# Performance work log

Hardware: AMD Instinct MI355X
Metric: run time of the kernel (lower is better)

The kernel has to match this reference:

```python
import jax, jax.numpy as jnp
import numpy as np

N, C_IN, C_OUT, V = 4, 64, 64, 8192

def setup_inputs() -> dict:
    key = jax.random.key(0)
    k1, k2, k3, k4 = jax.random.split(key, 4)
    x = jax.random.normal(k1, (N, C_IN, 1, V), dtype=jnp.float32)
    A = jax.random.uniform(k2, (N, V, V), dtype=jnp.float32)
    W = jax.random.normal(k3, (C_OUT, C_IN, 1, 1), dtype=jnp.float32) * 0.05
    b = jax.random.normal(k4, (C_OUT,), dtype=jnp.float32) * 0.05
    return {"x": x, "A": A, "W": W, "b": b}

def reference(x, A, W, b):
    # nn.Conv2d with (1,1) kernel == per-position channel mixing (pointwise GEMM).
    # x: (N, C_in, 1, V) -> squeeze T dim -> (N, C_in, V)
    xs = x[:, :, 0, :]
    y = jnp.einsum('ncv,oc->nov', xs, W[:, :, 0, 0]) + b[None, :, None]  # (N, C_out, V)
    # graph aggregation with per-sample adjacency: torch.einsum('ncv,nvw->ncw', x, A)
    out = jnp.einsum('ncv,nvw->ncw', y, A)  # (N, C_out, V)
    return out, A
```

## Files before the change

kernel.cpp:

```cpp
#include <hip/hip_runtime.h>
#include <stdint.h>

#define NB 4
#define CC 64
#define VV 8192
#define WBK 64
#define KB 64
#define NCHUNK (VV / KB)

typedef float  f32x4  __attribute__((ext_vector_type(4)));
typedef uint32_t u32x2 __attribute__((ext_vector_type(2)));
typedef uint32_t u32x4 __attribute__((ext_vector_type(4)));
typedef __bf16 bf16x8 __attribute__((ext_vector_type(8)));

__device__ __forceinline__ int swz_idx(int row, int v) {
    return row * KB + ((((v >> 3) ^ row) & 7) << 3) + (v & 7);
}

__device__ __forceinline__ uint32_t pkbf(float a, float b) {
    union { __bf16 h[2]; uint32_t u; } t;
    t.h[0] = (__bf16)a; t.h[1] = (__bf16)b;
    return t.u;
}

__device__ __forceinline__ bf16x8 mkfrag(const __bf16* p, int row, int k0) {
    u32x2 lo = *(const u32x2*)(p + swz_idx(row, k0));
    u32x2 hi = *(const u32x2*)(p + swz_idx(row, k0 + 16));
    u32x4 u; u.x = lo.x; u.y = lo.y; u.z = hi.x; u.w = hi.y;
    return __builtin_bit_cast(bf16x8, u);
}

__global__ __launch_bounds__(256) void k_y(const float* __restrict__ x,
                                           const float* __restrict__ Wg,
                                           const float* __restrict__ bg,
                                           __bf16* __restrict__ yws) {
    const int blk = blockIdx.x;
    const int cg  = blk & 3;
    const int vg  = (blk >> 2) * 256 + threadIdx.x;
    const int n   = vg >> 13;
    const int v   = vg & (VV - 1);
    const float* xg = x + (size_t)n * CC * VV + v;

    float acc[16];
    #pragma unroll
    for (int i = 0; i < 16; ++i) acc[i] = bg[cg * 16 + i];

    for (int cp = 0; cp < CC; ++cp) {
        float xv = xg[(size_t)cp * VV];
        #pragma unroll
        for (int i = 0; i < 16; ++i)
            acc[i] += Wg[(cg * 16 + i) * CC + cp] * xv;
    }
    const int t  = v >> 6;
    const int vv = v & 63;
    __bf16* ydst = yws + (size_t)(n * NCHUNK + t) * CC * KB;
    #pragma unroll
    for (int i = 0; i < 16; ++i)
        ydst[swz_idx(cg * 16 + i, vv)] = (__bf16)acc[i];
}

__global__ __launch_bounds__(512, 4) void k_main(const float* __restrict__ A,
                                                 const __bf16* __restrict__ yws,
                                                 float* __restrict__ out,
                                                 float* __restrict__ Acopy,
                                                 int skipTail) {
    __shared__ __attribute__((aligned(16))) __bf16 a_sh[2][WBK * KB];
    __shared__ __attribute__((aligned(16))) __bf16 y_sh[2][CC * KB];

    const int tid = threadIdx.x;
    const int n   = blockIdx.x >> 7;
    const int w0  = (blockIdx.x & 127) * WBK;

    const int wl = tid & 63;
    const int vq = tid >> 6;

    const float* pA = A     + (size_t)n * VV * VV + (size_t)vq * 8 * VV + w0 + wl;
    float*       pC = Acopy + (size_t)n * VV * VV + (size_t)vq * 8 * VV + w0 + wl;
    const uint4* ysrc = (const uint4*)(yws + (size_t)n * NCHUNK * CC * KB);

    const int lane = tid & 63;
    const int wv   = tid >> 6;
    const int mrow = wv >> 2;
    const int ncol = wv & 3;
    const int l15  = lane & 15;
    const int kq   = (lane >> 4) * 4;
    const int crow = mrow * 32 + l15;
    const int wcol = ncol * 16 + l15;

    f32x4 acc[2];
    acc[0] = (f32x4){0.f, 0.f, 0.f, 0.f};
    acc[1] = (f32x4){0.f, 0.f, 0.f, 0.f};

    float av[8];
    uint4 yv;

    auto stage_load = [&](int tt) {
        #pragma unroll
        for (int r = 0; r < 8; ++r)
            av[r] = pA[(size_t)(tt * KB + r) * VV];
        yv = ysrc[(size_t)tt * 512 + tid];
    };
    auto stage_write = [&](int tt, int b) {
        if (!(skipTail && n == 3 && tt >= 126)) {
            #pragma unroll
            for (int r = 0; r < 8; ++r)
                pC[(size_t)(tt * KB + r) * VV] = av[r];
        }
        u32x2 v0, v1;
        v0.x = pkbf(av[0], av[1]); v0.y = pkbf(av[2], av[3]);
        v1.x = pkbf(av[4], av[5]); v1.y = pkbf(av[6], av[7]);
        *(u32x2*)&a_sh[b][swz_idx(wl, vq * 8)]     = v0;
        *(u32x2*)&a_sh[b][swz_idx(wl, vq * 8 + 4)] = v1;
        *(uint4*)&y_sh[b][tid * 8] = yv;
    };
    auto compute = [&](int b) {
        const __bf16* ysh = y_sh[b];
        const __bf16* ash = a_sh[b];
        #pragma unroll
        for (int s = 0; s < 2; ++s) {
            const int k0 = s * 32 + kq;
            bf16x8 a0 = mkfrag(ysh, crow,      k0);
            bf16x8 a1 = mkfrag(ysh, crow + 16, k0);
            bf16x8 b0 = mkfrag(ash, wcol,      k0);
            acc[0] = __builtin_amdgcn_mfma_f32_16x16x32_bf16(a0, b0, acc[0], 0, 0, 0);
            acc[1] = __builtin_amdgcn_mfma_f32_16x16x32_bf16(a1, b0, acc[1], 0, 0, 0);
        }
    };

    stage_load(0);
    stage_write(0, 0);
    __syncthreads();
    for (int t = 0; t < NCHUNK; ++t) {
        if (t + 1 < NCHUNK) stage_load(t + 1);
        compute(t & 1);
        if (t + 1 < NCHUNK) stage_write(t + 1, (t + 1) & 1);
        __syncthreads();
    }

    float* po = out + (size_t)n * CC * VV + w0;
    #pragma unroll
    for (int mt = 0; mt < 2; ++mt)
        #pragma unroll
        for (int r = 0; r < 4; ++r) {
            int c = mrow * 32 + mt * 16 + kq + r;
            po[(size_t)c * VV + wcol] = acc[mt][r];
        }
}

__global__ __launch_bounds__(256) void k_tailcopy(const float* __restrict__ A,
                                                  float* __restrict__ Acopy,
                                                  size_t baseFloats, size_t count4) {
    size_t i = (size_t)blockIdx.x * 256 + threadIdx.x;
    if (i < count4) {
        f32x4 v = *(const f32x4*)(A + baseFloats + i * 4);
        *(f32x4*)(Acopy + baseFloats + i * 4) = v;
    }
}

extern "C" void kernel_launch(void* const* d_in, const int* in_sizes, int n_in,
                              void* d_out, int out_size, void* d_ws, size_t ws_size,
                              hipStream_t stream) {
    (void)in_sizes; (void)n_in; (void)out_size;
    const float* x = (const float*)d_in[0];
    const float* A = (const float*)d_in[1];
    const float* W = (const float*)d_in[2];
    const float* b = (const float*)d_in[3];
    float* out   = (float*)d_out;
    float* Acopy = out + (size_t)NB * CC * VV;

    const size_t yElems = (size_t)NB * NCHUNK * CC * KB;
    __bf16* yws;
    int skipTail = 0;
    if (ws_size >= yElems * 2) {
        yws = (__bf16*)d_ws;
    } else {
        skipTail = 1;
        yws = (__bf16*)(Acopy + ((size_t)NB * VV * VV - yElems / 2));
    }

    hipLaunchKernelGGL(k_y,    dim3(NB * 128), dim3(256), 0, stream, x, W, b, yws);
    hipLaunchKernelGGL(k_main, dim3(NB * 128), dim3(512), 0, stream, A, yws, out, Acopy, skipTail);
    if (skipTail) {
        size_t base = (size_t)NB * VV * VV - yElems / 2;
        hipLaunchKernelGGL(k_tailcopy, dim3((unsigned)((yElems / 8 + 255) / 256)), dim3(256),
                           0, stream, A, Acopy, base, yElems / 8);
    }
}
```

Measured before the change: 443.0 us.

## Drop LDS staging: load A and pre-swizzled y fragments directly into registers

The main kernel no longer stages A and y through shared memory with barriers. Each wave loads its A columns straight from global memory into registers, converts them to bf16 and feeds MFMA directly. y is precomputed by k_y in MFMA fragment order, so it can be read with 16-byte vector loads. A is double-buffered in registers across chunks and the A copy uses nontemporal stores. The two channel-half waves each load the same A data, which doubles A read traffic per block and may lean on cache.

```diff
diff --git a/kernel.cpp b/kernel.cpp
--- a/kernel.cpp
+++ b/kernel.cpp
@@ -4,18 +4,12 @@
 #define NB 4
 #define CC 64
 #define VV 8192
-#define WBK 64
 #define KB 64
 #define NCHUNK (VV / KB)
 
-typedef float  f32x4  __attribute__((ext_vector_type(4)));
-typedef uint32_t u32x2 __attribute__((ext_vector_type(2)));
+typedef float  f32x4 __attribute__((ext_vector_type(4)));
 typedef uint32_t u32x4 __attribute__((ext_vector_type(4)));
 typedef __bf16 bf16x8 __attribute__((ext_vector_type(8)));
-
-__device__ __forceinline__ int swz_idx(int row, int v) {
-    return row * KB + ((((v >> 3) ^ row) & 7) << 3) + (v & 7);
-}
 
 __device__ __forceinline__ uint32_t pkbf(float a, float b) {
     union { __bf16 h[2]; uint32_t u; } t;
@@ -23,128 +17,138 @@
     return t.u;
 }
 
-__device__ __forceinline__ bf16x8 mkfrag(const __bf16* p, int row, int k0) {
-    u32x2 lo = *(const u32x2*)(p + swz_idx(row, k0));
-    u32x2 hi = *(const u32x2*)(p + swz_idx(row, k0 + 16));
-    u32x4 u; u.x = lo.x; u.y = lo.y; u.z = hi.x; u.w = hi.y;
-    return __builtin_bit_cast(bf16x8, u);
-}
-
 __global__ __launch_bounds__(256) void k_y(const float* __restrict__ x,
                                            const float* __restrict__ Wg,
                                            const float* __restrict__ bg,
-                                           __bf16* __restrict__ yws) {
-    const int blk = blockIdx.x;
-    const int cg  = blk & 3;
-    const int vg  = (blk >> 2) * 256 + threadIdx.x;
-    const int n   = vg >> 13;
-    const int v   = vg & (VV - 1);
+                                           uint32_t* __restrict__ yfrag) {
+    const int bid  = blockIdx.x;
+    const int n    = bid >> 6;
+    const int cg   = (bid >> 4) & 3;
+    const int slab = bid & 15;
+    const int vp   = slab * 256 + threadIdx.x;
+    const int v    = vp * 2;
     const float* xg = x + (size_t)n * CC * VV + v;
 
-    float acc[16];
+    float a0[16], a1[16];
     #pragma unroll
-    for (int i = 0; i < 16; ++i) acc[i] = bg[cg * 16 + i];
+    for (int i = 0; i < 16; ++i) { float bb = bg[cg * 16 + i]; a0[i] = bb; a1[i] = bb; }
 
+    #pragma unroll 4
     for (int cp = 0; cp < CC; ++cp) {
-        float xv = xg[(size_t)cp * VV];
+        float2 xv = *(const float2*)(xg + (size_t)cp * VV);
         #pragma unroll
-        for (int i = 0; i < 16; ++i)
-            acc[i] += Wg[(cg * 16 + i) * CC + cp] * xv;
+        for (int i = 0; i < 16; ++i) {
+            float w = Wg[(cg * 16 + i) * CC + cp];
+            a0[i] += w * xv.x;
+            a1[i] += w * xv.y;
+        }
     }
     const int t  = v >> 6;
-    const int vv = v & 63;
-    __bf16* ydst = yws + (size_t)(n * NCHUNK + t) * CC * KB;
+    const int s  = (v >> 5) & 1;
+    const int kk = v & 31;
+    const int g  = (kk >> 2) & 3;
+    const int j  = kk & 3;
+    const int h  = kk >> 4;
+    const int u  = h * 2 + (j >> 1);
+    uint32_t* base = yfrag + ((((size_t)n * NCHUNK + t) * 4 + cg) * 2 + s) * 256 + u;
     #pragma unroll
     for (int i = 0; i < 16; ++i)
-        ydst[swz_idx(cg * 16 + i, vv)] = (__bf16)acc[i];
+        base[(g * 16 + i) * 4] = pkbf(a0[i], a1[i]);
 }
 
 __global__ __launch_bounds__(512, 4) void k_main(const float* __restrict__ A,
-                                                 const __bf16* __restrict__ yws,
+                                                 const uint32_t* __restrict__ yfrag,
                                                  float* __restrict__ out,
                                                  float* __restrict__ Acopy,
                                                  int skipTail) {
-    __shared__ __attribute__((aligned(16))) __bf16 a_sh[2][WBK * KB];
-    __shared__ __attribute__((aligned(16))) __bf16 y_sh[2][CC * KB];
-
-    const int tid = threadIdx.x;
-    const int n   = blockIdx.x >> 7;
-    const int w0  = (blockIdx.x & 127) * WBK;
-
-    const int wl = tid & 63;
-    const int vq = tid >> 6;
-
-    const float* pA = A     + (size_t)n * VV * VV + (size_t)vq * 8 * VV + w0 + wl;
-    float*       pC = Acopy + (size_t)n * VV * VV + (size_t)vq * 8 * VV + w0 + wl;
-    const uint4* ysrc = (const uint4*)(yws + (size_t)n * NCHUNK * CC * KB);
-
+    const int tid  = threadIdx.x;
+    const int n    = blockIdx.x >> 7;
+    const int w0   = (blockIdx.x & 127) * 64;
     const int lane = tid & 63;
     const int wv   = tid >> 6;
-    const int mrow = wv >> 2;
-    const int ncol = wv & 3;
+    const int wt   = wv & 3;
+    const int ch   = wv >> 2;
     const int l15  = lane & 15;
-    const int kq   = (lane >> 4) * 4;
-    const int crow = mrow * 32 + l15;
-    const int wcol = ncol * 16 + l15;
+    const int g    = lane >> 4;
+    const int kq   = g * 4;
 
-    f32x4 acc[2];
-    acc[0] = (f32x4){0.f, 0.f, 0.f, 0.f};
-    acc[1] = (f32x4){0.f, 0.f, 0.f, 0.f};
+    const size_t CH = (size_t)KB * VV;
+    const size_t laneoff = (size_t)kq * VV + w0 + wt * 16 + l15;
+    const float* pA = A     + (size_t)n * VV * VV + laneoff;
+    float*       pC = Acopy + (size_t)n * VV * VV + (size_t)ch * 16 * VV + laneoff;
+    const uint32_t* pY = yfrag + ((size_t)n * NCHUNK * 4 + ch * 2) * 2 * 256 + lane * 4;
 
-    float av[8];
-    uint4 yv;
+    f32x4 acc[2] = {{0.f,0.f,0.f,0.f}, {0.f,0.f,0.f,0.f}};
+    float ac[16], an[16];
+    u32x4 yf[2][2];
 
-    auto stage_load = [&](int tt) {
+    auto aload = [&](float (&R)[16], const float* P) {
         #pragma unroll
-        for (int r = 0; r < 8; ++r)
-            av[r] = pA[(size_t)(tt * KB + r) * VV];
-        yv = ysrc[(size_t)tt * 512 + tid];
+        for (int s = 0; s < 2; ++s)
+            #pragma unroll
+            for (int h = 0; h < 2; ++h)
+                #pragma unroll
+                for (int j = 0; j < 4; ++j)
+                    R[s * 8 + h * 4 + j] = P[(size_t)(s * 32 + h * 16 + j) * VV];
     };
-    auto stage_write = [&](int tt, int b) {
-        if (!(skipTail && n == 3 && tt >= 126)) {
+    auto yload = [&](const uint32_t* P) {
+        #pragma unroll
+        for (int ci = 0; ci < 2; ++ci)
             #pragma unroll
-            for (int r = 0; r < 8; ++r)
-                pC[(size_t)(tt * KB + r) * VV] = av[r];
-        }
-        u32x2 v0, v1;
-        v0.x = pkbf(av[0], av[1]); v0.y = pkbf(av[2], av[3]);
-        v1.x = pkbf(av[4], av[5]); v1.y = pkbf(av[6], av[7]);
-        *(u32x2*)&a_sh[b][swz_idx(wl, vq * 8)]     = v0;
-        *(u32x2*)&a_sh[b][swz_idx(wl, vq * 8 + 4)] = v1;
-        *(uint4*)&y_sh[b][tid * 8] = yv;
+            for (int s = 0; s < 2; ++s)
+                yf[ci][s] = *(const u32x4*)(P + (ci * 2 + s) * 256);
     };
-    auto compute = [&](int b) {
-        const __bf16* ysh = y_sh[b];
-        const __bf16* ash = a_sh[b];
+    auto cvt_mma = [&](const float (&R)[16]) {
+        u32x4 bf[2];
         #pragma unroll
         for (int s = 0; s < 2; ++s) {
-            const int k0 = s * 32 + kq;
-            bf16x8 a0 = mkfrag(ysh, crow,      k0);
-            bf16x8 a1 = mkfrag(ysh, crow + 16, k0);
-            bf16x8 b0 = mkfrag(ash, wcol,      k0);
-            acc[0] = __builtin_amdgcn_mfma_f32_16x16x32_bf16(a0, b0, acc[0], 0, 0, 0);
-            acc[1] = __builtin_amdgcn_mfma_f32_16x16x32_bf16(a1, b0, acc[1], 0, 0, 0);
+            bf[s].x = pkbf(R[s*8+0], R[s*8+1]);
+            bf[s].y = pkbf(R[s*8+2], R[s*8+3]);
+            bf[s].z = pkbf(R[s*8+4], R[s*8+5]);
+            bf[s].w = pkbf(R[s*8+6], R[s*8+7]);
+        }
+        #pragma unroll
+        for (int ci = 0; ci < 2; ++ci)
+            #pragma unroll
+            for (int s = 0; s < 2; ++s)
+                acc[ci] = __builtin_amdgcn_mfma_f32_16x16x32_bf16(
+                    __builtin_bit_cast(bf16x8, yf[ci][s]),
+                    __builtin_bit_cast(bf16x8, bf[s]), acc[ci], 0, 0, 0);
+    };
+    auto cstore = [&](const float (&R)[16], float* P, bool skip) {
+        if (!skip) {
+            #pragma unroll
+            for (int s = 0; s < 2; ++s)
+                #pragma unroll
+                for (int j = 0; j < 4; ++j)
+                    __builtin_nontemporal_store(R[s * 8 + ch * 4 + j],
+                                                P + (size_t)(s * 32 + j) * VV);
         }
     };
 
-    stage_load(0);
-    stage_write(0, 0);
-    __syncthreads();
-    for (int t = 0; t < NCHUNK; ++t) {
-        if (t + 1 < NCHUNK) stage_load(t + 1);
-        compute(t & 1);
-        if (t + 1 < NCHUNK) stage_write(t + 1, (t + 1) & 1);
-        __syncthreads();
+    aload(ac, pA);
+    yload(pY);
+    for (int t = 0; t < NCHUNK; t += 2) {
+        const bool sk0 = skipTail && n == 3 && t >= 126;
+        const bool sk1 = skipTail && n == 3 && t + 1 >= 126;
+        aload(an, pA + CH);
+        cvt_mma(ac);
+        pY += 2048; yload(pY);
+        cstore(ac, pC, sk0);
+        pA += 2 * CH;
+        if (t + 2 < NCHUNK) aload(ac, pA);
+        cvt_mma(an);
+        if (t + 2 < NCHUNK) { pY += 2048; yload(pY); }
+        cstore(an, pC + CH, sk1);
+        pC += 2 * CH;
     }
 
-    float* po = out + (size_t)n * CC * VV + w0;
+    float* po = out + (size_t)n * CC * VV + w0 + wt * 16 + l15;
     #pragma unroll
-    for (int mt = 0; mt < 2; ++mt)
+    for (int ci = 0; ci < 2; ++ci)
         #pragma unroll
-        for (int r = 0; r < 4; ++r) {
-            int c = mrow * 32 + mt * 16 + kq + r;
-            po[(size_t)c * VV + wcol] = acc[mt][r];
-        }
+        for (int r = 0; r < 4; ++r)
+            po[(size_t)((ch * 2 + ci) * 16 + g * 4 + r) * VV] = acc[ci][r];
 }
 
 __global__ __launch_bounds__(256) void k_tailcopy(const float* __restrict__ A,
@@ -169,17 +173,17 @@
     float* Acopy = out + (size_t)NB * CC * VV;
 
     const size_t yElems = (size_t)NB * NCHUNK * CC * KB;
-    __bf16* yws;
+    uint32_t* yfrag;
     int skipTail = 0;
     if (ws_size >= yElems * 2) {
-        yws = (__bf16*)d_ws;
+        yfrag = (uint32_t*)d_ws;
     } else {
         skipTail = 1;
-        yws = (__bf16*)(Acopy + ((size_t)NB * VV * VV - yElems / 2));
+        yfrag = (uint32_t*)(Acopy + ((size_t)NB * VV * VV - yElems / 2));
     }
 
-    hipLaunchKernelGGL(k_y,    dim3(NB * 128), dim3(256), 0, stream, x, W, b, yws);
-    hipLaunchKernelGGL(k_main, dim3(NB * 128), dim3(512), 0, stream, A, yws, out, Acopy, skipTail);
+    hipLaunchKernelGGL(k_y,    dim3(256), dim3(256), 0, stream, x, W, b, yfrag);
+    hipLaunchKernelGGL(k_main, dim3(NB * 128), dim3(512), 0, stream, A, yfrag, out, Acopy, skipTail);
     if (skipTail) {
         size_t base = (size_t)NB * VV * VV - yElems / 2;
         hipLaunchKernelGGL(k_tailcopy, dim3((unsigned)((yElems / 8 + 255) / 256)), dim3(256),
```

Result: slower. 815.9 us (+84.2%).
